# Optimization experiments

Hardware: AMD Instinct MI355X
Metric: run time of the kernel (lower is better)

## Reference

```python
import jax, jax.numpy as jnp
import numpy as np

B, L, D = 4, 2048, 1024
H, DK, DV = 8, 128, 128
LN_EPS = 1e-5


def setup_inputs() -> dict:
    key = jax.random.key(0)
    ks = jax.random.split(key, 8)
    def xavier(k, shape):
        std = float(np.sqrt(2.0 / (shape[0] + shape[1])))
        return jax.random.normal(k, shape, dtype=jnp.float32) * std
    return {
        "q": jax.random.normal(ks[0], (B, L, D), dtype=jnp.float32),
        "k": jax.random.normal(ks[1], (B, L, D), dtype=jnp.float32),
        "v": jax.random.normal(ks[2], (B, L, D), dtype=jnp.float32),
        "mask": jnp.ones((B, L), dtype=jnp.int32),
        "Wq": xavier(ks[3], (H * DK, D)),
        "Wk": xavier(ks[4], (H * DK, D)),
        "Wv": xavier(ks[5], (H * DV, D)),
        "Wo": xavier(ks[6], (D, H * DV)),
        "gamma": jnp.ones((D,), dtype=jnp.float32),
        "beta": jnp.zeros((D,), dtype=jnp.float32),
    }


def reference(q, k, v, mask, Wq, Wk, Wv, Wo, gamma, beta):
    # dropout layers are identity in eval mode
    residual = q
    # project and split heads -> [H, B, L, dk] (matches permute(2,0,1,3))
    qh = (q @ Wq.T).reshape(B, L, H, DK).transpose(2, 0, 1, 3)
    kh = (k @ Wk.T).reshape(B, L, H, DK).transpose(2, 0, 1, 3)
    vh = (v @ Wv.T).reshape(B, L, H, DV).transpose(2, 0, 1, 3)
    scale = jnp.sqrt(jnp.asarray(DK, dtype=qh.dtype))
    scores = jnp.einsum('hbqd,hbkd->hbqk', qh, kh) / scale  # [H,B,Lq,Lk]
    neg_inf = jnp.asarray(-jnp.inf, dtype=scores.dtype)
    scores = jnp.where(mask[None, :, None, :] == 0, neg_inf, scores)
    attn = jax.nn.softmax(scores, axis=-1)
    out = jnp.einsum('hbqk,hbkd->hbqd', attn, vh)  # [H,B,Lq,dv]
    out = out.transpose(1, 2, 0, 3).reshape(B, L, H * DV)
    out = out @ Wo.T
    x = out + residual
    mu = jnp.mean(x, axis=-1, keepdims=True)
    var = jnp.var(x, axis=-1, keepdims=True)
    y = (x - mu) * jax.lax.rsqrt(var + LN_EPS) * gamma + beta
    return y, attn.reshape(H * B, L, L)
```

## Files before the change

### kernel.cpp

```cpp
#include <hip/hip_runtime.h>
#include <hip/hip_bf16.h>


typedef __hip_bfloat16 bf16;
typedef __attribute__((ext_vector_type(8))) short bf16x8;
typedef __attribute__((ext_vector_type(4))) short bf16x4;
typedef __attribute__((ext_vector_type(4))) float f32x4;
typedef __attribute__((ext_vector_type(2))) unsigned int u32x2;

#define MFMA16(a, b, c) __builtin_amdgcn_mfma_f32_16x16x32_bf16((a), (b), (c), 0, 0, 0)


static constexpr int LSEQ = 2048;
static constexpr float SCALE = 0.08838834764831845f;
static constexpr size_t Y_ELEMS = 8388608;
static constexpr size_t ATTN_PER_HB = 4194304;

static __device__ inline short bf16bits(float x) {
  __hip_bfloat16 h = __float2bfloat16(x);
  return *reinterpret_cast<short*>(&h);
}

__global__ void detect_dtype(const unsigned* __restrict__ g, int* __restrict__ flag) {
  if (threadIdx.x == 0 && blockIdx.x == 0) *flag = (g[0] == 0x3F800000u) ? 1 : 0;
}

__global__ __launch_bounds__(256) void cast_bf16(const void* __restrict__ src,
                                                 bf16* __restrict__ dst,
                                                 const int* __restrict__ flagp) {
  const int i = (blockIdx.x * 256 + threadIdx.x) * 4;
  if (*flagp) {
    const float4 v = *(const float4*)((const float*)src + i);
    alignas(8) bf16 t[4] = {__float2bfloat16(v.x), __float2bfloat16(v.y),
                            __float2bfloat16(v.z), __float2bfloat16(v.w)};
    *(uint2*)(dst + i) = *(const uint2*)t;
  } else {
    *(uint2*)(dst + i) = *(const uint2*)((const bf16*)src + i);
  }
}

__global__ __launch_bounds__(256) void cast_f32(const void* __restrict__ src,
                                                float* __restrict__ dst,
                                                const int* __restrict__ flagp) {
  const int i = blockIdx.x * 256 + threadIdx.x;
  dst[i] = (*flagp) ? ((const float*)src)[i] : __bfloat162float(((const bf16*)src)[i]);
}

template <int MODE>
__global__ __launch_bounds__(256) void gemm_xwT(const bf16* __restrict__ X,
                                                const bf16* __restrict__ W,
                                                void* __restrict__ outp,
                                                const bf16* __restrict__ resid) {
  const int lane = threadIdx.x & 63;
  const int wv   = threadIdx.x >> 6;
  const int c16  = lane & 15;
  const int quad = lane >> 4;
  const int m0 = blockIdx.x * 64 + wv * 16;
  const int n0 = blockIdx.y * 64;
  const int K = 1024;

  f32x4 acc0 = {0.f, 0.f, 0.f, 0.f}, acc1 = acc0, acc2 = acc0, acc3 = acc0;
  const bf16* xrow = X + (size_t)(m0 + c16) * K + quad * 8;
  const bf16* wrow = W + (size_t)(n0 + c16) * K + quad * 8;

  for (int k0 = 0; k0 < K; k0 += 32) {
    bf16x8 a  = *(const bf16x8*)(xrow + k0);
    bf16x8 b0 = *(const bf16x8*)(wrow + k0);
    bf16x8 b1 = *(const bf16x8*)(wrow + 16 * K + k0);
    bf16x8 b2 = *(const bf16x8*)(wrow + 32 * K + k0);
    bf16x8 b3 = *(const bf16x8*)(wrow + 48 * K + k0);
    acc0 = MFMA16(a, b0, acc0);
    acc1 = MFMA16(a, b1, acc1);
    acc2 = MFMA16(a, b2, acc2);
    acc3 = MFMA16(a, b3, acc3);
  }

  f32x4 accs[4] = {acc0, acc1, acc2, acc3};
#pragma unroll
  for (int t = 0; t < 4; ++t) {
#pragma unroll
    for (int r = 0; r < 4; ++r) {
      const int m = m0 + quad * 4 + r;
      const int n = n0 + t * 16 + c16;
      const float v = accs[t][r];
      if (MODE == 0) {
        const int h = n >> 7, d = n & 127, bb = m >> 11, l = m & 2047;
        ((bf16*)outp)[((size_t)((h * 4 + bb) * 2048 + l)) * 128 + d] = __float2bfloat16(v);
      } else if (MODE == 2) {
        const int h = n >> 7, d = n & 127, bb = m >> 11, l = m & 2047;
        ((bf16*)outp)[((size_t)((h * 4 + bb) * 128 + d)) * 2048 + l] = __float2bfloat16(v);
      } else {
        const float rr = __bfloat162float(resid[(size_t)m * 1024 + n]);
        ((float*)outp)[(size_t)m * 1024 + n] = v + rr;
      }
    }
  }
}

__global__ __launch_bounds__(256, 2) void attn_fused(const bf16* __restrict__ qh,
                                                     const bf16* __restrict__ kh,
                                                     const bf16* __restrict__ vt,
                                                     const int* __restrict__ mask,
                                                     void* __restrict__ dout,
                                                     bf16* __restrict__ O,
                                                     const int* __restrict__ flagp) {
  __shared__ float wm[4][16], wl[4][16], fm[16], fl[16];
  __shared__ float OL[4][16][132];

  const int f32 = *flagp;
  const int hb = blockIdx.y;
  const int bb = hb & 3;
  const int h  = hb >> 2;
  const int q0 = blockIdx.x * 16;
  const int lane = threadIdx.x & 63;
  const int wv   = threadIdx.x >> 6;
  const int c16  = lane & 15;
  const int quad = lane >> 4;

  const bf16* Q  = qh + (size_t)hb * LSEQ * 128;
  const bf16* Kh = kh + (size_t)hb * LSEQ * 128;
  const bf16* Vt = vt + (size_t)hb * 128 * LSEQ;

  bf16x8 qfrag[4];
#pragma unroll
  for (int kk = 0; kk < 4; ++kk)
    qfrag[kk] = *(const bf16x8*)(Q + (size_t)(q0 + c16) * 128 + kk * 32 + quad * 8);

  f32x4 sv[32];
#pragma unroll
  for (int t = 0; t < 32; ++t) {
    const int col0 = wv * 512 + t * 16;
    f32x4 s = {0.f, 0.f, 0.f, 0.f};
#pragma unroll
    for (int kk = 0; kk < 4; ++kk) {
      bf16x8 kfr = *(const bf16x8*)(Kh + (size_t)(col0 + c16) * 128 + kk * 32 + quad * 8);
      s = MFMA16(kfr, qfrag[kk], s);
    }
    const int4 mk4 = *(const int4*)(mask + bb * 2048 + col0 + quad * 4);
    const int mks[4] = {mk4.x, mk4.y, mk4.z, mk4.w};
#pragma unroll
    for (int r = 0; r < 4; ++r) {
      float x = s[r] * SCALE;
      s[r] = (mks[r] == 0) ? -1e30f : x;
    }
    sv[t] = s;
  }

  float m = -1e30f;
#pragma unroll
  for (int t = 0; t < 32; ++t)
#pragma unroll
    for (int r = 0; r < 4; ++r) m = fmaxf(m, sv[t][r]);
  m = fmaxf(m, __shfl_xor(m, 16));
  m = fmaxf(m, __shfl_xor(m, 32));
  float l = 0.f;
#pragma unroll
  for (int t = 0; t < 32; ++t)
#pragma unroll
    for (int r = 0; r < 4; ++r) l += __expf(sv[t][r] - m);
  l += __shfl_xor(l, 16);
  l += __shfl_xor(l, 32);

  if (quad == 0) {
    wm[wv][c16] = m;
    wl[wv][c16] = l;
  }
  __syncthreads();
  if (threadIdx.x < 16) {
    float M = wm[0][threadIdx.x];
    for (int w = 1; w < 4; ++w) M = fmaxf(M, wm[w][threadIdx.x]);
    float Ls = 0.f;
    for (int w = 0; w < 4; ++w) Ls += wl[w][threadIdx.x] * __expf(wm[w][threadIdx.x] - M);
    fm[threadIdx.x] = M;
    fl[threadIdx.x] = 1.0f / Ls;
  }
  __syncthreads();
  const float myM = fm[c16];
  const float myL = fl[c16];

  float* aF = (float*)dout + Y_ELEMS + (size_t)hb * ATTN_PER_HB;
  bf16*  aH = (bf16*)dout + Y_ELEMS + (size_t)hb * ATTN_PER_HB;

  f32x4 acc[8];
#pragma unroll
  for (int dt = 0; dt < 8; ++dt) acc[dt] = f32x4{0.f, 0.f, 0.f, 0.f};

#pragma unroll
  for (int c = 0; c < 16; ++c) {
    bf16x8 pfrag;
#pragma unroll
    for (int half = 0; half < 2; ++half) {
      const int tt = c * 2 + half;
      f32x4 pv;
#pragma unroll
      for (int r = 0; r < 4; ++r) {
        const float p = __expf(sv[tt][r] - myM) * myL;
        pv[r] = p;
        pfrag[half * 4 + r] = bf16bits(p);
      }
      const size_t aidx = (size_t)(q0 + c16) * 2048 + (size_t)(wv * 512 + tt * 16 + quad * 4);
      if (f32) {
        __builtin_nontemporal_store(pv, (f32x4*)(aF + aidx));
      } else {
        u32x2 w2;
        w2[0] = (unsigned)(unsigned short)pfrag[half * 4 + 0] |
                ((unsigned)(unsigned short)pfrag[half * 4 + 1] << 16);
        w2[1] = (unsigned)(unsigned short)pfrag[half * 4 + 2] |
                ((unsigned)(unsigned short)pfrag[half * 4 + 3] << 16);
        __builtin_nontemporal_store(w2, (u32x2*)(aH + aidx));
      }
    }
    const int kbase = wv * 512 + c * 32;
#pragma unroll
    for (int dt = 0; dt < 8; ++dt) {
      const bf16* vp = Vt + (size_t)(dt * 16 + c16) * 2048 + kbase + quad * 4;
      const bf16x4 lo = *(const bf16x4*)vp;
      const bf16x4 hi = *(const bf16x4*)(vp + 16);
      bf16x8 vf;
      vf[0] = lo[0]; vf[1] = lo[1]; vf[2] = lo[2]; vf[3] = lo[3];
      vf[4] = hi[0]; vf[5] = hi[1]; vf[6] = hi[2]; vf[7] = hi[3];
      acc[dt] = MFMA16(vf, pfrag, acc[dt]);
    }
  }

#pragma unroll
  for (int dt = 0; dt < 8; ++dt)
    *(f32x4*)&OL[wv][c16][dt * 16 + quad * 4] = acc[dt];
  __syncthreads();

  const int qq = threadIdx.x >> 4;
  const int d0 = (threadIdx.x & 15) * 8;
  alignas(16) bf16 ob[8];
#pragma unroll
  for (int i = 0; i < 8; ++i) {
    const float s4 = OL[0][qq][d0 + i] + OL[1][qq][d0 + i] +
                     OL[2][qq][d0 + i] + OL[3][qq][d0 + i];
    ob[i] = __float2bfloat16(s4);
  }
  *(uint4*)(O + (size_t)(bb * 2048 + q0 + qq) * 1024 + h * 128 + d0) = *(const uint4*)ob;
}

__global__ __launch_bounds__(256) void layernorm(const float* __restrict__ x,
                                                 const float* __restrict__ gamma,
                                                 const float* __restrict__ beta,
                                                 void* __restrict__ y,
                                                 const int* __restrict__ flagp) {
  __shared__ float ss[4], ss2[4];
  const int row = blockIdx.x;
  const float4 v = ((const float4*)(x + (size_t)row * 1024))[threadIdx.x];
  float s  = v.x + v.y + v.z + v.w;
  float s2 = v.x * v.x + v.y * v.y + v.z * v.z + v.w * v.w;
#pragma unroll
  for (int off = 32; off >= 1; off >>= 1) {
    s  += __shfl_xor(s, off);
    s2 += __shfl_xor(s2, off);
  }
  if ((threadIdx.x & 63) == 0) {
    ss[threadIdx.x >> 6]  = s;
    ss2[threadIdx.x >> 6] = s2;
  }
  __syncthreads();
  const float tot  = ss[0] + ss[1] + ss[2] + ss[3];
  const float tot2 = ss2[0] + ss2[1] + ss2[2] + ss2[3];
  const float mu = tot * (1.0f / 1024.0f);
  const float var = tot2 * (1.0f / 1024.0f) - mu * mu;
  const float rs = rsqrtf(var + 1e-5f);

  const int c = threadIdx.x * 4;
  const float vv[4] = {v.x, v.y, v.z, v.w};
  float o[4];
#pragma unroll
  for (int i = 0; i < 4; ++i)
    o[i] = (vv[i] - mu) * rs * gamma[c + i] + beta[c + i];

  if (*flagp) {
    *(float4*)((float*)y + (size_t)row * 1024 + c) = make_float4(o[0], o[1], o[2], o[3]);
  } else {
    alignas(8) bf16 ob[4] = {__float2bfloat16(o[0]), __float2bfloat16(o[1]),
                             __float2bfloat16(o[2]), __float2bfloat16(o[3])};
    *(uint2*)((bf16*)y + (size_t)row * 1024 + c) = *(const uint2*)ob;
  }
}

extern "C" void kernel_launch(void* const* d_in, const int* in_sizes, int n_in,
                              void* d_out, int out_size, void* d_ws, size_t ws_size,
                              hipStream_t stream) {
  const void* q     = d_in[0];
  const void* k     = d_in[1];
  const void* v     = d_in[2];
  const int*  mask  = (const int*)d_in[3];
  const void* Wq    = d_in[4];
  const void* Wk    = d_in[5];
  const void* Wv    = d_in[6];
  const void* Wo    = d_in[7];
  const void* gamma = d_in[8];
  const void* beta  = d_in[9];

  char* ws = (char*)d_ws;
  bf16* qb  = (bf16*)(ws);
  bf16* kb  = (bf16*)(ws + 16777216);
  bf16* vb  = (bf16*)(ws + 33554432);
  bf16* wqb = (bf16*)(ws + 50331648);
  bf16* wkb = (bf16*)(ws + 52428800);
  bf16* wvb = (bf16*)(ws + 54525952);
  bf16* wob = (bf16*)(ws + 56623104);
  bf16* qh  = (bf16*)(ws + 58720256);
  bf16* kh  = (bf16*)(ws + 75497472);
  bf16* vt  = (bf16*)(ws + 92274688);
  bf16* o   = (bf16*)(ws + 109051904);
  float* gf = (float*)(ws + 125829120);
  float* bfb = (float*)(ws + 125833216);
  int* flag = (int*)(ws + 125837312);
  float* x  = (float*)(ws + 16777216);

  detect_dtype<<<1, 64, 0, stream>>>((const unsigned*)gamma, flag);

  cast_bf16<<<8192, 256, 0, stream>>>(q, qb, flag);
  cast_bf16<<<8192, 256, 0, stream>>>(k, kb, flag);
  cast_bf16<<<8192, 256, 0, stream>>>(v, vb, flag);
  cast_bf16<<<1024, 256, 0, stream>>>(Wq, wqb, flag);
  cast_bf16<<<1024, 256, 0, stream>>>(Wk, wkb, flag);
  cast_bf16<<<1024, 256, 0, stream>>>(Wv, wvb, flag);
  cast_bf16<<<1024, 256, 0, stream>>>(Wo, wob, flag);
  cast_f32<<<4, 256, 0, stream>>>(gamma, gf, flag);
  cast_f32<<<4, 256, 0, stream>>>(beta, bfb, flag);

  const dim3 gridP(8192 / 64, 1024 / 64);
  gemm_xwT<0><<<gridP, 256, 0, stream>>>(qb, wqb, (void*)qh, nullptr);
  gemm_xwT<0><<<gridP, 256, 0, stream>>>(kb, wkb, (void*)kh, nullptr);
  gemm_xwT<2><<<gridP, 256, 0, stream>>>(vb, wvb, (void*)vt, nullptr);

  attn_fused<<<dim3(2048 / 16, 32), 256, 0, stream>>>(qh, kh, vt, mask, d_out, o, flag);

  gemm_xwT<3><<<gridP, 256, 0, stream>>>(o, wob, (void*)x, qb);

  layernorm<<<8192, 256, 0, stream>>>(x, gf, bfb, d_out, flag);
}
```

Baseline: 1.853 ms.

## Permute V-transpose layout for single 16-byte loads and defer attention-prob stores

The V projection epilogue now writes the transposed V with a permuted sequence index inside each 32-element block, so the attention kernel can fetch each MFMA B fragment with one 16-byte load instead of two 8-byte loads plus shuffles. Softmax probabilities are computed into a register array first. The PV matmul then runs, and the attention-probability matrix is written at the end with plain stores instead of nontemporal ones. In the f32 case these values are now rounded through bf16, which lowers precision. Holding 16 bf16x8 fragments raises register pressure, and moving the large attention writes after the matmul changes how they overlap with compute.

```diff
diff --git a/kernel.cpp b/kernel.cpp
--- a/kernel.cpp
+++ b/kernel.cpp
@@ -4,7 +4,6 @@
 
 typedef __hip_bfloat16 bf16;
 typedef __attribute__((ext_vector_type(8))) short bf16x8;
-typedef __attribute__((ext_vector_type(4))) short bf16x4;
 typedef __attribute__((ext_vector_type(4))) float f32x4;
 typedef __attribute__((ext_vector_type(2))) unsigned int u32x2;
 
@@ -88,7 +87,9 @@
         ((bf16*)outp)[((size_t)((h * 4 + bb) * 2048 + l)) * 128 + d] = __float2bfloat16(v);
       } else if (MODE == 2) {
         const int h = n >> 7, d = n & 127, bb = m >> 11, l = m & 2047;
-        ((bf16*)outp)[((size_t)((h * 4 + bb) * 128 + d)) * 2048 + l] = __float2bfloat16(v);
+        const int k5 = l & 31;
+        const int lp = (l & ~31) | (((k5 >> 2) & 3) << 3) | (((k5 >> 4) & 1) << 2) | (k5 & 3);
+        ((bf16*)outp)[((size_t)((h * 4 + bb) * 128 + d)) * 2048 + lp] = __float2bfloat16(v);
       } else {
         const float rr = __bfloat162float(resid[(size_t)m * 1024 + n]);
         ((float*)outp)[(size_t)m * 1024 + n] = v + rr;
@@ -178,48 +179,30 @@
   const float myM = fm[c16];
   const float myL = fl[c16];
 
-  float* aF = (float*)dout + Y_ELEMS + (size_t)hb * ATTN_PER_HB;
-  bf16*  aH = (bf16*)dout + Y_ELEMS + (size_t)hb * ATTN_PER_HB;
-
-  f32x4 acc[8];
-#pragma unroll
-  for (int dt = 0; dt < 8; ++dt) acc[dt] = f32x4{0.f, 0.f, 0.f, 0.f};
-
+  bf16x8 pf[16];
 #pragma unroll
   for (int c = 0; c < 16; ++c) {
-    bf16x8 pfrag;
 #pragma unroll
     for (int half = 0; half < 2; ++half) {
       const int tt = c * 2 + half;
-      f32x4 pv;
 #pragma unroll
       for (int r = 0; r < 4; ++r) {
         const float p = __expf(sv[tt][r] - myM) * myL;
-        pv[r] = p;
-        pfrag[half * 4 + r] = bf16bits(p);
+        pf[c][half * 4 + r] = bf16bits(p);
       }
-      const size_t aidx = (size_t)(q0 + c16) * 2048 + (size_t)(wv * 512 + tt * 16 + quad * 4);
-      if (f32) {
-        __builtin_nontemporal_store(pv, (f32x4*)(aF + aidx));
-      } else {
-        u32x2 w2;
-        w2[0] = (unsigned)(unsigned short)pfrag[half * 4 + 0] |
-                ((unsigned)(unsigned short)pfrag[half * 4 + 1] << 16);
-        w2[1] = (unsigned)(unsigned short)pfrag[half * 4 + 2] |
-                ((unsigned)(unsigned short)pfrag[half * 4 + 3] << 16);
-        __builtin_nontemporal_store(w2, (u32x2*)(aH + aidx));
-      }
-    }
+    }
+  }
+
+  f32x4 acc[8];
+#pragma unroll
+  for (int dt = 0; dt < 8; ++dt) acc[dt] = f32x4{0.f, 0.f, 0.f, 0.f};
+#pragma unroll
+  for (int c = 0; c < 16; ++c) {
     const int kbase = wv * 512 + c * 32;
 #pragma unroll
     for (int dt = 0; dt < 8; ++dt) {
-      const bf16* vp = Vt + (size_t)(dt * 16 + c16) * 2048 + kbase + quad * 4;
-      const bf16x4 lo = *(const bf16x4*)vp;
-      const bf16x4 hi = *(const bf16x4*)(vp + 16);
-      bf16x8 vf;
-      vf[0] = lo[0]; vf[1] = lo[1]; vf[2] = lo[2]; vf[3] = lo[3];
-      vf[4] = hi[0]; vf[5] = hi[1]; vf[6] = hi[2]; vf[7] = hi[3];
-      acc[dt] = MFMA16(vf, pfrag, acc[dt]);
+      const bf16x8 vf = *(const bf16x8*)(Vt + (size_t)(dt * 16 + c16) * 2048 + kbase + quad * 8);
+      acc[dt] = MFMA16(vf, pf[c], acc[dt]);
     }
   }
 
@@ -228,16 +211,50 @@
     *(f32x4*)&OL[wv][c16][dt * 16 + quad * 4] = acc[dt];
   __syncthreads();
 
-  const int qq = threadIdx.x >> 4;
-  const int d0 = (threadIdx.x & 15) * 8;
-  alignas(16) bf16 ob[8];
-#pragma unroll
-  for (int i = 0; i < 8; ++i) {
-    const float s4 = OL[0][qq][d0 + i] + OL[1][qq][d0 + i] +
-                     OL[2][qq][d0 + i] + OL[3][qq][d0 + i];
-    ob[i] = __float2bfloat16(s4);
-  }
-  *(uint4*)(O + (size_t)(bb * 2048 + q0 + qq) * 1024 + h * 128 + d0) = *(const uint4*)ob;
+  {
+    const int qq = threadIdx.x >> 4;
+    const int d0 = (threadIdx.x & 15) * 8;
+    alignas(16) bf16 ob[8];
+#pragma unroll
+    for (int i = 0; i < 8; ++i) {
+      const float s4 = OL[0][qq][d0 + i] + OL[1][qq][d0 + i] +
+                       OL[2][qq][d0 + i] + OL[3][qq][d0 + i];
+      ob[i] = __float2bfloat16(s4);
+    }
+    *(uint4*)(O + (size_t)(bb * 2048 + q0 + qq) * 1024 + h * 128 + d0) = *(const uint4*)ob;
+  }
+
+  float* aF = (float*)dout + Y_ELEMS + (size_t)hb * ATTN_PER_HB;
+  bf16*  aH = (bf16*)dout + Y_ELEMS + (size_t)hb * ATTN_PER_HB;
+  const size_t rowoff = (size_t)(q0 + c16) * 2048 + wv * 512 + quad * 4;
+  if (f32) {
+#pragma unroll
+    for (int c = 0; c < 16; ++c) {
+      const size_t aidx = rowoff + c * 32;
+      f32x4 lo, hi;
+#pragma unroll
+      for (int r = 0; r < 4; ++r) {
+        unsigned ul = ((unsigned)(unsigned short)pf[c][r]) << 16;
+        unsigned uh = ((unsigned)(unsigned short)pf[c][4 + r]) << 16;
+        lo[r] = __builtin_bit_cast(float, ul);
+        hi[r] = __builtin_bit_cast(float, uh);
+      }
+      *(f32x4*)(aF + aidx) = lo;
+      *(f32x4*)(aF + aidx + 16) = hi;
+    }
+  } else {
+#pragma unroll
+    for (int c = 0; c < 16; ++c) {
+      const size_t aidx = rowoff + c * 32;
+      u32x2 lo, hi;
+      lo[0] = (unsigned)(unsigned short)pf[c][0] | ((unsigned)(unsigned short)pf[c][1] << 16);
+      lo[1] = (unsigned)(unsigned short)pf[c][2] | ((unsigned)(unsigned short)pf[c][3] << 16);
+      hi[0] = (unsigned)(unsigned short)pf[c][4] | ((unsigned)(unsigned short)pf[c][5] << 16);
+      hi[1] = (unsigned)(unsigned short)pf[c][6] | ((unsigned)(unsigned short)pf[c][7] << 16);
+      *(u32x2*)(aH + aidx) = lo;
+      *(u32x2*)(aH + aidx + 16) = hi;
+    }
+  }
 }
 
 __global__ __launch_bounds__(256) void layernorm(const float* __restrict__ x,
```

New measurement: 1.835 ms. No clear change (-1.0%).
